# Kernel tuning notes

Measured on AMD Instinct MI355X. Metric: run time of the kernel, lower is better.

Reference implementation:

```python
import jax, jax.numpy as jnp
import numpy as np

D_MODEL = 1024
N_HEADS = 16
D_K = 64
B = 2
S = 2048


def setup_inputs() -> dict:
    key = jax.random.key(0)
    ks = jax.random.split(key, 6)
    scale = 1.0 / np.sqrt(D_MODEL)
    x = jax.random.normal(ks[0], (B, S, D_MODEL), dtype=jnp.float32)
    Wq = jax.random.normal(ks[1], (D_MODEL, D_MODEL), dtype=jnp.float32) * scale
    Wk = jax.random.normal(ks[2], (D_MODEL, D_MODEL), dtype=jnp.float32) * scale
    Wv = jax.random.normal(ks[3], (D_MODEL, D_MODEL), dtype=jnp.float32) * scale
    Wo = jax.random.normal(ks[4], (D_MODEL, D_MODEL), dtype=jnp.float32) * scale
    bq = jnp.zeros((D_MODEL,), jnp.float32)
    bk = jnp.zeros((D_MODEL,), jnp.float32)
    bv = jnp.zeros((D_MODEL,), jnp.float32)
    bo = jnp.zeros((D_MODEL,), jnp.float32)
    # causal mask, broadcast over batch and heads: [1, 1, S, S]
    mask = jnp.tril(jnp.ones((S, S), jnp.int32))[None, None, :, :]
    return {"x": x, "mask": mask, "Wq": Wq, "bq": bq, "Wk": Wk, "bk": bk,
            "Wv": Wv, "bv": bv, "Wo": Wo, "bo": bo}


def reference(x, mask, Wq, bq, Wk, bk, Wv, bv, Wo, bo):
    b, s, _ = x.shape
    # projections (torch Linear: y = x @ W^T + b); split heads -> [b, h, s, d_k]
    def split_heads(y):
        return y.reshape(b, s, N_HEADS, D_K).transpose(0, 2, 1, 3)
    Q = split_heads(x @ Wq.T + bq)
    K = split_heads(x @ Wk.T + bk)
    V = split_heads(x @ Wv.T + bv)
    scores = jnp.einsum('bhqd,bhkd->bhqk', Q, K) / jnp.sqrt(jnp.float32(D_K))
    scores = jnp.where(mask == 0, -jnp.inf, scores)
    attn = jax.nn.softmax(scores, axis=-1)  # dropout p=0 -> identity
    out = jnp.einsum('bhqk,bhkd->bhqd', attn, V)
    out = out.transpose(0, 2, 1, 3).reshape(b, s, D_MODEL)
    return out @ Wo.T + bo
```

## Files before the change

### kernel.cpp

```cpp
#include <hip/hip_runtime.h>
#include <math.h>
#include <type_traits>

#define D_MODEL 1024
#define N_HEADS 16
#define D_KK    64
#define B_SZ    2
#define SEQ     2048
#define M_TOTAL (B_SZ * SEQ)

#define QSCALE 0.18033688011112042f
#define FIXM 12.0f

typedef __attribute__((ext_vector_type(8)))  short short8;
typedef __attribute__((ext_vector_type(4)))  float f32x4;
typedef __attribute__((ext_vector_type(16))) float f32x16;

static __device__ __forceinline__ ushort f2bf(float f) {
    union { float f; unsigned u; } c; c.f = f;
    unsigned u = c.u;
    unsigned r = (u + 0x7fffu + ((u >> 16) & 1u)) >> 16;
    return (ushort)r;
}

static __device__ __forceinline__ unsigned cvtpk(float a, float b) {
    unsigned r;
    asm("v_cvt_pk_bf16_f32 %0, %1, %2" : "=v"(r) : "v"(a), "v"(b));
    return r;
}
static __device__ __forceinline__ void pswap(unsigned &a, unsigned &b) {
    asm("v_permlane32_swap_b32 %0, %1" : "+v"(a), "+v"(b));
}

static __device__ __forceinline__ void gload16(const void* g, void* l) {
    __builtin_amdgcn_global_load_lds(
        (const __attribute__((address_space(1))) void*)g,
        (__attribute__((address_space(3))) void*)l, 16, 0, 0);
}

__global__ __launch_bounds__(256)
void cvt_kernel(const float* __restrict__ x,  const float* __restrict__ wq,
                const float* __restrict__ wk, const float* __restrict__ wv,
                const float* __restrict__ wo,
                ushort* __restrict__ xb,  ushort* __restrict__ wqb,
                ushort* __restrict__ wkb, ushort* __restrict__ wvb,
                ushort* __restrict__ wob)
{
    const float* s; ushort* d; int n4;
    switch (blockIdx.y) {
        case 0:  s = x;  d = xb;  n4 = M_TOTAL * D_MODEL / 4; break;
        case 1:  s = wq; d = wqb; n4 = D_MODEL * D_MODEL / 4; break;
        case 2:  s = wk; d = wkb; n4 = D_MODEL * D_MODEL / 4; break;
        case 3:  s = wv; d = wvb; n4 = D_MODEL * D_MODEL / 4; break;
        default: s = wo; d = wob; n4 = D_MODEL * D_MODEL / 4; break;
    }
    const int stride = gridDim.x * blockDim.x;
    for (int i = blockIdx.x * blockDim.x + threadIdx.x; i < n4; i += stride) {
        float4 v = reinterpret_cast<const float4*>(s)[i];
        ushort4 u;
        u.x = f2bf(v.x); u.y = f2bf(v.y); u.z = f2bf(v.z); u.w = f2bf(v.w);
        reinterpret_cast<ushort4*>(d)[i] = u;
    }
}

template<int EPI>
__global__ __launch_bounds__(256)
void gemm_mfma(const ushort* __restrict__ A,
               const ushort* __restrict__ W0, const float* __restrict__ b0, void* __restrict__ C0,
               const ushort* __restrict__ W1, const float* __restrict__ b1, void* __restrict__ C1,
               const ushort* __restrict__ W2, const float* __restrict__ b2, void* __restrict__ C2)
{
    constexpr int K = D_MODEL;

    __shared__ ushort As[2][128 * 64];
    __shared__ ushort Bs[2][64 * 64];

    const int id  = blockIdx.x;
    const int xcd = id & 7;
    const int j   = id >> 3;
    const int mt  = xcd * 4 + (j & 3);
    const int ntz = j >> 2;
    const int nt  = ntz & 15;
    const int z   = ntz >> 4;

    const ushort* W    = W0;
    const float*  bias = b0;
    void*         C    = C0;
    if (z == 1) { W = W1; bias = b1; C = C1; }
    else if (z == 2) { W = W2; bias = b2; C = C2; }

    const int m0 = mt * 128;
    const int n0 = nt * 64;

    const int tid  = threadIdx.x;
    const int w    = tid >> 6;
    const int lane = tid & 63;
    const int lr   = lane & 15;
    const int lc   = lane >> 4;
    const int wr   = w >> 1;
    const int wc   = w & 1;

    const int rsub = lane >> 3;
    const int csw  = ((lane & 7) ^ rsub) << 3;

    const ushort* gA = A + (size_t)(m0 + w * 8 + rsub) * K + csw;
    const ushort* gB = W + (size_t)(n0 + w * 8 + rsub) * K + csw;

    f32x4 acc[4][2];
#pragma unroll
    for (int m = 0; m < 4; ++m)
#pragma unroll
        for (int n = 0; n < 2; ++n) acc[m][n] = (f32x4)0.0f;

#pragma unroll
    for (int ca = 0; ca < 4; ++ca)
        gload16(gA + (size_t)(32 * ca) * K, &As[0][(w + 4 * ca) * 512]);
#pragma unroll
    for (int cb = 0; cb < 2; ++cb)
        gload16(gB + (size_t)(32 * cb) * K, &Bs[0][(w + 4 * cb) * 512]);
    __syncthreads();

    const int swz = (lr & 7) << 4;
    int buf = 0;
    for (int it = 0; it < 16; ++it) {
        if (it < 15) {
            const int kn = (it + 1) * 64;
#pragma unroll
            for (int ca = 0; ca < 4; ++ca)
                gload16(gA + (size_t)(32 * ca) * K + kn, &As[buf ^ 1][(w + 4 * ca) * 512]);
#pragma unroll
            for (int cb = 0; cb < 2; ++cb)
                gload16(gB + (size_t)(32 * cb) * K + kn, &Bs[buf ^ 1][(w + 4 * cb) * 512]);
        }

        short8 af[4][2], bfr[2][2];
#pragma unroll
        for (int m = 0; m < 4; ++m) {
            const int rbyte = (wr * 64 + m * 16 + lr) * 128;
#pragma unroll
            for (int kk = 0; kk < 2; ++kk)
                af[m][kk] = *reinterpret_cast<const short8*>(
                    &As[buf][(rbyte + ((kk * 64 + lc * 16) ^ swz)) >> 1]);
        }
#pragma unroll
        for (int n = 0; n < 2; ++n) {
            const int rbyte = (wc * 32 + n * 16 + lr) * 128;
#pragma unroll
            for (int kk = 0; kk < 2; ++kk)
                bfr[n][kk] = *reinterpret_cast<const short8*>(
                    &Bs[buf][(rbyte + ((kk * 64 + lc * 16) ^ swz)) >> 1]);
        }
#pragma unroll
        for (int kk = 0; kk < 2; ++kk)
#pragma unroll
            for (int m = 0; m < 4; ++m)
#pragma unroll
                for (int n = 0; n < 2; ++n)
                    acc[m][n] = __builtin_amdgcn_mfma_f32_16x16x32_bf16(
                        af[m][kk], bfr[n][kk], acc[m][n], 0, 0, 0);

        __syncthreads();
        buf ^= 1;
    }

    float bv[2];
#pragma unroll
    for (int n = 0; n < 2; ++n) bv[n] = bias[n0 + wc * 32 + n * 16 + lr];
    const int row_base = m0 + wr * 64;

    if (EPI == 0) {
        float* Cf = (float*)C;
#pragma unroll
        for (int m = 0; m < 4; ++m)
#pragma unroll
        for (int r = 0; r < 4; ++r) {
            const int row = row_base + m * 16 + lc * 4 + r;
#pragma unroll
            for (int n = 0; n < 2; ++n)
                Cf[(size_t)row * D_MODEL + n0 + wc * 32 + n * 16 + lr] =
                    acc[m][n][r] + bv[n];
        }
    } else {
        ushort* Cu = (ushort*)C;
        const bool vt   = (z == 2);
        const float osc = (z == 0) ? QSCALE : 1.0f;
#pragma unroll
        for (int m = 0; m < 4; ++m) {
            const int row4 = row_base + m * 16 + lc * 4;
            const int bb = row4 >> 11;
            const int ss = row4 & 2047;
            const size_t bhbase = (size_t)bb * N_HEADS;
#pragma unroll
            for (int n = 0; n < 2; ++n) {
                const int col = n0 + wc * 32 + n * 16 + lr;
                const int h = col >> 6, d = col & 63;
                if (vt) {
                    ushort4 u;
                    u.x = f2bf(acc[m][n][0] + bv[n]);
                    u.y = f2bf(acc[m][n][1] + bv[n]);
                    u.z = f2bf(acc[m][n][2] + bv[n]);
                    u.w = f2bf(acc[m][n][3] + bv[n]);
                    *reinterpret_cast<ushort4*>(
                        &Cu[((bhbase + h) * D_KK + d) * SEQ + ss]) = u;
                } else {
#pragma unroll
                    for (int r = 0; r < 4; ++r)
                        Cu[((bhbase + h) * SEQ + ss + r) * D_KK + d] =
                            f2bf((acc[m][n][r] + bv[n]) * osc);
                }
            }
        }
    }
}

__global__ __launch_bounds__(256, 2)
void attn_mfma_kernel(const ushort* __restrict__ Qb, const ushort* __restrict__ Kb,
                      const ushort* __restrict__ Vt, ushort* __restrict__ Ob)
{
    __shared__ ushort Ks[2][4096];
    __shared__ ushort Vs[2][4096];

    const int tid  = threadIdx.x;
    const int w    = tid >> 6;
    const int lane = tid & 63;
    const int l31  = lane & 31;
    const int hi   = lane >> 5;
    const int swl  = (lane & 7) << 4;

    const int id  = blockIdx.x;
    const int xcd = id & 7;
    const int j   = id >> 3;
    const int bh  = xcd * 4 + (j & 3);
    const int qx  = j >> 2;
    const int b   = bh >> 4;
    const int h   = bh & 15;

    const int myqb = (w < 2) ? qx : (31 - qx);
    const int qw0  = myqb * 64 + (w & 1) * 32;
    const int qr   = (w & 1) * 32 + l31;
    const int ntmx = 32 - qx;

    const ushort* Kbase = Kb + (size_t)bh * SEQ * D_KK;
    const ushort* Vbase = Vt + (size_t)bh * D_KK * SEQ;

    const int rsub = lane >> 3;
    const int csw  = ((lane & 7) ^ rsub) << 3;

    auto stage = [&](int kofs, int s) {
#pragma unroll
        for (int cc = 0; cc < 2; ++cc) {
            const int c = w + cc * 4;
            gload16(Kbase + (size_t)(kofs + c * 8 + rsub) * D_KK + csw,
                    &Ks[s][c * 512]);
            gload16(Vbase + (size_t)(c * 8 + rsub) * SEQ + kofs + csw,
                    &Vs[s][c * 512]);
        }
    };

    auto makefrag = [&](const f32x16& sv, int o) -> short8 {
        unsigned u0 = cvtpk(sv[o + 0], sv[o + 1]);
        unsigned u1 = cvtpk(sv[o + 2], sv[o + 3]);
        unsigned u2 = cvtpk(sv[o + 4], sv[o + 5]);
        unsigned u3 = cvtpk(sv[o + 6], sv[o + 7]);
        pswap(u0, u2);
        pswap(u1, u3);
        int4 t = make_int4((int)u0, (int)u1, (int)u2, (int)u3);
        return *reinterpret_cast<short8*>(&t);
    };

    const ushort* Qp = Qb + ((size_t)bh * SEQ + qw0 + l31) * D_KK + 8 * hi;
    short8 qf[4];
#pragma unroll
    for (int ds = 0; ds < 4; ++ds)
        qf[ds] = *reinterpret_cast<const short8*>(Qp + 16 * ds);

    f32x16 ot0 = (f32x16)0.0f, ot1 = (f32x16)0.0f;
    float l_run = 0.0f;

    stage(0, 0);
    __syncthreads();

    int buf = 0;
    for (int it = 0; it < ntmx; ++it) {
        if (it + 1 < ntmx) stage((it + 1) * 64, buf ^ 1);

        if (it <= myqb) {
            const ushort* Ksb = &Ks[buf][0];
            const ushort* Vsb = &Vs[buf][0];

            f32x16 s0 = (f32x16)0.0f, s1 = (f32x16)0.0f;
#pragma unroll
            for (int ds = 0; ds < 4; ++ds) {
                const int cb = (32 * ds + 16 * hi) ^ swl;
                const short8 a0 = *reinterpret_cast<const short8*>(
                    &Ksb[(l31 * 128 + cb) >> 1]);
                const short8 a1 = *reinterpret_cast<const short8*>(
                    &Ksb[((32 + l31) * 128 + cb) >> 1]);
                s0 = __builtin_amdgcn_mfma_f32_32x32x16_bf16(a0, qf[ds], s0, 0, 0, 0);
                s1 = __builtin_amdgcn_mfma_f32_32x32x16_bf16(a1, qf[ds], s1, 0, 0, 0);
            }

            if (it == myqb) {
#pragma unroll
                for (int reg = 0; reg < 16; ++reg) {
                    const int k32 = (reg & 3) + 8 * (reg >> 2) + 4 * hi;
                    if (k32 > qr)      s0[reg] = -1e30f;
                    if (k32 + 32 > qr) s1[reg] = -1e30f;
                }
            }

            float rsum = 0.0f;
#pragma unroll
            for (int reg = 0; reg < 16; ++reg) {
                const float p0 = __builtin_amdgcn_exp2f(s0[reg] - FIXM);
                const float p1 = __builtin_amdgcn_exp2f(s1[reg] - FIXM);
                s0[reg] = p0; s1[reg] = p1;
                rsum += p0 + p1;
            }
            l_run += rsum;

            const short8 pb0 = makefrag(s0, 0);
            const short8 pb1 = makefrag(s0, 8);
            const short8 pb2 = makefrag(s1, 0);
            const short8 pb3 = makefrag(s1, 8);

#pragma unroll
            for (int dg = 0; dg < 2; ++dg) {
                const int row = dg * 32 + l31;
                f32x16& ot = dg ? ot1 : ot0;
#pragma unroll
                for (int ks = 0; ks < 4; ++ks) {
                    const int cb = (32 * ks + 16 * hi) ^ swl;
                    const short8 vf = *reinterpret_cast<const short8*>(
                        &Vsb[(row * 128 + cb) >> 1]);
                    const short8 pb = (ks == 0) ? pb0 : (ks == 1) ? pb1
                                     : (ks == 2) ? pb2 : pb3;
                    ot = __builtin_amdgcn_mfma_f32_32x32x16_bf16(vf, pb, ot, 0, 0, 0);
                }
            }
        }

        __syncthreads();
        buf ^= 1;
    }

    const float l_tot = l_run + __shfl_xor(l_run, 32);
    const float linv  = 1.0f / l_tot;
    ushort* Op = Ob + ((size_t)b * SEQ + qw0 + l31) * D_MODEL + h * D_KK;
#pragma unroll
    for (int dg = 0; dg < 2; ++dg) {
        const f32x16& ot = dg ? ot1 : ot0;
#pragma unroll
        for (int m = 0; m < 4; ++m) {
            ushort4 u;
            u.x = f2bf(ot[4 * m + 0] * linv);
            u.y = f2bf(ot[4 * m + 1] * linv);
            u.z = f2bf(ot[4 * m + 2] * linv);
            u.w = f2bf(ot[4 * m + 3] * linv);
            *reinterpret_cast<ushort4*>(&Op[dg * 32 + m * 8 + 4 * hi]) = u;
        }
    }
}

extern "C" void kernel_launch(void* const* d_in, const int* in_sizes, int n_in,
                              void* d_out, int out_size, void* d_ws, size_t ws_size,
                              hipStream_t stream)
{
    const float* x  = (const float*)d_in[0];
    const float* Wq = (const float*)d_in[2];
    const float* bq = (const float*)d_in[3];
    const float* Wk = (const float*)d_in[4];
    const float* bk = (const float*)d_in[5];
    const float* Wv = (const float*)d_in[6];
    const float* bv = (const float*)d_in[7];
    const float* Wo = (const float*)d_in[8];
    const float* bo = (const float*)d_in[9];
    float* out = (float*)d_out;

    const size_t TSZ = (size_t)M_TOTAL * D_MODEL;
    const size_t WSZ = (size_t)D_MODEL * D_MODEL;
    ushort* xb  = (ushort*)d_ws;
    ushort* Wqb = xb  + TSZ;
    ushort* Wkb = Wqb + WSZ;
    ushort* Wvb = Wkb + WSZ;
    ushort* Wob = Wvb + WSZ;
    ushort* Qb  = Wob + WSZ;
    ushort* Kb  = Qb  + TSZ;
    ushort* Vt  = Kb  + TSZ;
    ushort* Ob  = Vt  + TSZ;

    dim3 blk(256);
    cvt_kernel<<<dim3(256, 5), blk, 0, stream>>>(x, Wq, Wk, Wv, Wo,
                                                 xb, Wqb, Wkb, Wvb, Wob);

    gemm_mfma<1><<<dim3(1536), blk, 0, stream>>>(xb, Wqb, bq, Qb,
                                                     Wkb, bk, Kb,
                                                     Wvb, bv, Vt);

    attn_mfma_kernel<<<dim3(512), blk, 0, stream>>>(Qb, Kb, Vt, Ob);

    gemm_mfma<0><<<dim3(512), blk, 0, stream>>>(Ob, Wob, bo, out,
                                                    Wob, bo, out,
                                                    Wob, bo, out);
}
```

Measured before the change: 107.2 us.

## Use single-wave attention blocks loading K/V fragments directly from global memory

The attention kernel drops its shared-memory double-buffered K/V staging and 4-wave blocks. Each block is now one 64-thread wave handling 32 query rows, with K and V MFMA fragments loaded straight from global memory into registers. The grid grows from 512 to 2048 blocks, scheduled heaviest-first, so there are no block barriers or idle waves on causal boundaries. The cost is that K/V are no longer shared across waves in LDS, so global and L2 traffic rises and load latency is exposed without explicit prefetch.

```diff
diff --git a/kernel.cpp b/kernel.cpp
--- a/kernel.cpp
+++ b/kernel.cpp
@@ -213,49 +213,28 @@
     }
 }
 
-__global__ __launch_bounds__(256, 2)
+__global__ __launch_bounds__(64)
 void attn_mfma_kernel(const ushort* __restrict__ Qb, const ushort* __restrict__ Kb,
                       const ushort* __restrict__ Vt, ushort* __restrict__ Ob)
 {
-    __shared__ ushort Ks[2][4096];
-    __shared__ ushort Vs[2][4096];
-
-    const int tid  = threadIdx.x;
-    const int w    = tid >> 6;
-    const int lane = tid & 63;
+    const int lane = threadIdx.x;
     const int l31  = lane & 31;
     const int hi   = lane >> 5;
-    const int swl  = (lane & 7) << 4;
 
     const int id  = blockIdx.x;
     const int xcd = id & 7;
-    const int j   = id >> 3;
-    const int bh  = xcd * 4 + (j & 3);
-    const int qx  = j >> 2;
+    const int r   = id >> 3;
+    const int bh  = xcd * 4 + (r & 3);
+    const int qi  = 63 - (r >> 2);
     const int b   = bh >> 4;
     const int h   = bh & 15;
 
-    const int myqb = (w < 2) ? qx : (31 - qx);
-    const int qw0  = myqb * 64 + (w & 1) * 32;
-    const int qr   = (w & 1) * 32 + l31;
-    const int ntmx = 32 - qx;
+    const int q0   = qi * 32;
+    const int nt   = (qi >> 1) + 1;
+    const int qrel = ((qi & 1) << 5) + l31;
 
     const ushort* Kbase = Kb + (size_t)bh * SEQ * D_KK;
     const ushort* Vbase = Vt + (size_t)bh * D_KK * SEQ;
-
-    const int rsub = lane >> 3;
-    const int csw  = ((lane & 7) ^ rsub) << 3;
-
-    auto stage = [&](int kofs, int s) {
-#pragma unroll
-        for (int cc = 0; cc < 2; ++cc) {
-            const int c = w + cc * 4;
-            gload16(Kbase + (size_t)(kofs + c * 8 + rsub) * D_KK + csw,
-                    &Ks[s][c * 512]);
-            gload16(Vbase + (size_t)(c * 8 + rsub) * SEQ + kofs + csw,
-                    &Vs[s][c * 512]);
-        }
-    };
 
     auto makefrag = [&](const f32x16& sv, int o) -> short8 {
         unsigned u0 = cvtpk(sv[o + 0], sv[o + 1]);
@@ -268,7 +247,7 @@
         return *reinterpret_cast<short8*>(&t);
     };
 
-    const ushort* Qp = Qb + ((size_t)bh * SEQ + qw0 + l31) * D_KK + 8 * hi;
+    const ushort* Qp = Qb + ((size_t)bh * SEQ + q0 + l31) * D_KK + 8 * hi;
     short8 qf[4];
 #pragma unroll
     for (int ds = 0; ds < 4; ++ds)
@@ -277,76 +256,67 @@
     f32x16 ot0 = (f32x16)0.0f, ot1 = (f32x16)0.0f;
     float l_run = 0.0f;
 
-    stage(0, 0);
-    __syncthreads();
-
-    int buf = 0;
-    for (int it = 0; it < ntmx; ++it) {
-        if (it + 1 < ntmx) stage((it + 1) * 64, buf ^ 1);
-
-        if (it <= myqb) {
-            const ushort* Ksb = &Ks[buf][0];
-            const ushort* Vsb = &Vs[buf][0];
-
-            f32x16 s0 = (f32x16)0.0f, s1 = (f32x16)0.0f;
-#pragma unroll
-            for (int ds = 0; ds < 4; ++ds) {
-                const int cb = (32 * ds + 16 * hi) ^ swl;
-                const short8 a0 = *reinterpret_cast<const short8*>(
-                    &Ksb[(l31 * 128 + cb) >> 1]);
-                const short8 a1 = *reinterpret_cast<const short8*>(
-                    &Ksb[((32 + l31) * 128 + cb) >> 1]);
-                s0 = __builtin_amdgcn_mfma_f32_32x32x16_bf16(a0, qf[ds], s0, 0, 0, 0);
-                s1 = __builtin_amdgcn_mfma_f32_32x32x16_bf16(a1, qf[ds], s1, 0, 0, 0);
+    for (int it = 0; it < nt; ++it) {
+        const int k0 = it * 64;
+
+        const ushort* Kr = Kbase + (size_t)(k0 + l31) * D_KK + 8 * hi;
+        short8 ka0[4], ka1[4];
+#pragma unroll
+        for (int ds = 0; ds < 4; ++ds) {
+            ka0[ds] = *reinterpret_cast<const short8*>(Kr + 16 * ds);
+            ka1[ds] = *reinterpret_cast<const short8*>(Kr + 32 * D_KK + 16 * ds);
+        }
+        const ushort* Vr = Vbase + (size_t)l31 * SEQ + k0 + 8 * hi;
+        short8 vf0[4], vf1[4];
+#pragma unroll
+        for (int ks = 0; ks < 4; ++ks) {
+            vf0[ks] = *reinterpret_cast<const short8*>(Vr + 16 * ks);
+            vf1[ks] = *reinterpret_cast<const short8*>(Vr + (size_t)32 * SEQ + 16 * ks);
+        }
+
+        f32x16 s0 = (f32x16)0.0f, s1 = (f32x16)0.0f;
+#pragma unroll
+        for (int ds = 0; ds < 4; ++ds) {
+            s0 = __builtin_amdgcn_mfma_f32_32x32x16_bf16(ka0[ds], qf[ds], s0, 0, 0, 0);
+            s1 = __builtin_amdgcn_mfma_f32_32x32x16_bf16(ka1[ds], qf[ds], s1, 0, 0, 0);
+        }
+
+        if (it == nt - 1) {
+#pragma unroll
+            for (int reg = 0; reg < 16; ++reg) {
+                const int k32 = (reg & 3) + 8 * (reg >> 2) + 4 * hi;
+                if (k32 > qrel)      s0[reg] = -1e30f;
+                if (k32 + 32 > qrel) s1[reg] = -1e30f;
             }
-
-            if (it == myqb) {
-#pragma unroll
-                for (int reg = 0; reg < 16; ++reg) {
-                    const int k32 = (reg & 3) + 8 * (reg >> 2) + 4 * hi;
-                    if (k32 > qr)      s0[reg] = -1e30f;
-                    if (k32 + 32 > qr) s1[reg] = -1e30f;
-                }
-            }
-
-            float rsum = 0.0f;
-#pragma unroll
-            for (int reg = 0; reg < 16; ++reg) {
-                const float p0 = __builtin_amdgcn_exp2f(s0[reg] - FIXM);
-                const float p1 = __builtin_amdgcn_exp2f(s1[reg] - FIXM);
-                s0[reg] = p0; s1[reg] = p1;
-                rsum += p0 + p1;
-            }
-            l_run += rsum;
-
-            const short8 pb0 = makefrag(s0, 0);
-            const short8 pb1 = makefrag(s0, 8);
-            const short8 pb2 = makefrag(s1, 0);
-            const short8 pb3 = makefrag(s1, 8);
-
-#pragma unroll
-            for (int dg = 0; dg < 2; ++dg) {
-                const int row = dg * 32 + l31;
-                f32x16& ot = dg ? ot1 : ot0;
-#pragma unroll
-                for (int ks = 0; ks < 4; ++ks) {
-                    const int cb = (32 * ks + 16 * hi) ^ swl;
-                    const short8 vf = *reinterpret_cast<const short8*>(
-                        &Vsb[(row * 128 + cb) >> 1]);
-                    const short8 pb = (ks == 0) ? pb0 : (ks == 1) ? pb1
-                                     : (ks == 2) ? pb2 : pb3;
-                    ot = __builtin_amdgcn_mfma_f32_32x32x16_bf16(vf, pb, ot, 0, 0, 0);
-                }
-            }
-        }
-
-        __syncthreads();
-        buf ^= 1;
+        }
+
+        float rsum = 0.0f;
+#pragma unroll
+        for (int reg = 0; reg < 16; ++reg) {
+            const float p0 = __builtin_amdgcn_exp2f(s0[reg] - FIXM);
+            const float p1 = __builtin_amdgcn_exp2f(s1[reg] - FIXM);
+            s0[reg] = p0; s1[reg] = p1;
+            rsum += p0 + p1;
+        }
+        l_run += rsum;
+
+        const short8 pb0 = makefrag(s0, 0);
+        const short8 pb1 = makefrag(s0, 8);
+        const short8 pb2 = makefrag(s1, 0);
+        const short8 pb3 = makefrag(s1, 8);
+
+#pragma unroll
+        for (int ks = 0; ks < 4; ++ks) {
+            const short8 pb = (ks == 0) ? pb0 : (ks == 1) ? pb1
+                             : (ks == 2) ? pb2 : pb3;
+            ot0 = __builtin_amdgcn_mfma_f32_32x32x16_bf16(vf0[ks], pb, ot0, 0, 0, 0);
+            ot1 = __builtin_amdgcn_mfma_f32_32x32x16_bf16(vf1[ks], pb, ot1, 0, 0, 0);
+        }
     }
 
     const float l_tot = l_run + __shfl_xor(l_run, 32);
     const float linv  = 1.0f / l_tot;
-    ushort* Op = Ob + ((size_t)b * SEQ + qw0 + l31) * D_MODEL + h * D_KK;
+    ushort* Op = Ob + ((size_t)b * SEQ + q0 + l31) * D_MODEL + h * D_KK;
 #pragma unroll
     for (int dg = 0; dg < 2; ++dg) {
         const f32x16& ot = dg ? ot1 : ot0;
@@ -397,7 +367,7 @@
                                                      Wkb, bk, Kb,
                                                      Wvb, bv, Vt);
 
-    attn_mfma_kernel<<<dim3(512), blk, 0, stream>>>(Qb, Kb, Vt, Ob);
+    attn_mfma_kernel<<<dim3(2048), dim3(64), 0, stream>>>(Qb, Kb, Vt, Ob);
 
     gemm_mfma<0><<<dim3(512), blk, 0, stream>>>(Ob, Wob, bo, out,
                                                     Wob, bo, out,
```

New measurement: 135.0 us. 25.9% more time.
